# Kernel tuning notes

Hardware: AMD Instinct MI355X
Metric: run time of the kernel (lower is better)

The kernel has to match this reference:

```python
import jax, jax.numpy as jnp
import numpy as np
import math

K_SLOTS = 64
DIM = 512
HEADS = 8
HEAD_DIM = DIM // HEADS
EPS = 1e-20
LN_EPS = 1e-5
SQRT_DIM = 1.0 / math.sqrt(HEAD_DIM)


def layernorm(x, g, b):
    mu = jnp.mean(x, axis=-1, keepdims=True)
    var = jnp.var(x, axis=-1, keepdims=True)
    return (x - mu) * jax.lax.rsqrt(var + LN_EPS) * g + b


def setup_inputs() -> dict:
    key = jax.random.key(0)
    ks = jax.random.split(key, 8)
    B, T = 8, 8192
    lim = 1.0 / math.sqrt(DIM)
    return {
        "X": jax.random.normal(ks[0], (B, T, DIM), jnp.float32),
        "slots_w": jax.random.normal(ks[1], (K_SLOTS, DIM), jnp.float32),
        "g_slots": jnp.ones((DIM,), jnp.float32),
        "b_slots": jnp.zeros((DIM,), jnp.float32),
        "Wk": jax.random.uniform(ks[2], (DIM, DIM), jnp.float32, -lim, lim),
        "bk": jax.random.uniform(ks[3], (DIM,), jnp.float32, -lim, lim),
        "Wv": jax.random.uniform(ks[4], (DIM, DIM), jnp.float32, -lim, lim),
        "bv": jax.random.uniform(ks[5], (DIM,), jnp.float32, -lim, lim),
        "g_after": jnp.ones((DIM,), jnp.float32),
        "b_after": jnp.zeros((DIM,), jnp.float32),
    }


def reference(X, slots_w, g_slots, b_slots, Wk, bk, Wv, bv, g_after, b_after):
    B, T, D = X.shape
    # slots -> queries, shared across batch: (K, D) -> (H, K, hd)
    S = layernorm(slots_w, g_slots, b_slots)
    Q = S.reshape(K_SLOTS, HEADS, HEAD_DIM).transpose(1, 0, 2)  # (H, K, hd)
    # key/value projections, head split: (B, T, D) -> (B, H, T, hd)
    Kx = (X @ Wk.T + bk).reshape(B, T, HEADS, HEAD_DIM).transpose(0, 2, 1, 3)
    V = (X @ Wv.T + bv).reshape(B, T, HEADS, HEAD_DIM).transpose(0, 2, 1, 3)
    # attention logits (B, H, K, T), scale = 1/sqrt(head_dim)
    A = jnp.einsum("hkd,bhsd->bhks", Q, Kx) * SQRT_DIM
    # softmax over the SLOT axis (k), then renormalize by row-sum over s
    W = jax.nn.softmax(A, axis=-2)
    C = jnp.sum(W, axis=-1, keepdims=True)  # (B, H, K, 1)
    A = W / (C + EPS)
    S_hat = jnp.einsum("bhks,bhsd->bhkd", A, V)  # (B, H, K, hd)
    S_hat = S_hat.transpose(0, 2, 1, 3).reshape(B, K_SLOTS, D)
    return layernorm(S_hat, g_after, b_after)
```

## Files before the change

kernel.cpp:

```cpp
#include <hip/hip_runtime.h>
#include <hip/hip_bf16.h>
#include <math.h>

typedef unsigned short ushort_t;
typedef unsigned int u32;

constexpr int D  = 512;
constexpr int T  = 8192;
constexpr int B  = 8;
constexpr int H  = 8;
constexpr int KS = 64;
constexpr int HD = 64;
constexpr float SCALE = 0.125f;
constexpr float LNEPS = 1e-5f;
constexpr float EPS   = 1e-20f;

constexpr int TC  = 128;
constexpr int CPB = 2;

constexpr size_t OFF_S    = 0;
constexpr size_t OFF_BQ   = 32768;
constexpr size_t OFF_SACC = 33280;
constexpr size_t OFF_CACC = 295424;
constexpr size_t OFF_WB2  = 299520;

typedef __attribute__((ext_vector_type(8))) short bf16x8;
typedef __attribute__((ext_vector_type(4))) float f32x4;
typedef __attribute__((ext_vector_type(4))) unsigned short us4;

typedef const __attribute__((address_space(1))) u32* gas_ptr;
typedef __attribute__((address_space(3))) u32* las_ptr;

__device__ __forceinline__ void gload16(const void* g, void* l) {
  __builtin_amdgcn_global_load_lds((gas_ptr)g, (las_ptr)l, 16, 0, 0);
}

__device__ __forceinline__ ushort_t f2bf(float x) {
  __hip_bfloat16 t = __float2bfloat16(x);
  return *(ushort_t*)&t;
}

__device__ __forceinline__ u32 pk2bf(float x, float y) {
  __hip_bfloat162 t = __float22bfloat162_rn(make_float2(x, y));
  return *(u32*)&t;
}

__device__ __forceinline__ bf16x8 cvt8(f32x4 a, f32x4 b) {
  union { bf16x8 v; u32 u[4]; } r;
  r.u[0] = pk2bf(a.x, a.y); r.u[1] = pk2bf(a.z, a.w);
  r.u[2] = pk2bf(b.x, b.y); r.u[3] = pk2bf(b.z, b.w);
  return r.v;
}

__global__ void ln_slots_kernel(const float* __restrict__ slots_w,
                                const float* __restrict__ g, const float* __restrict__ b,
                                const float* __restrict__ bk,
                                float* __restrict__ S, float* __restrict__ bq) {
  __shared__ float red[8];
  int k = blockIdx.x;
  int tid = threadIdx.x;
  float x0 = slots_w[k*D + tid];
  float x1 = slots_w[k*D + tid + 256];
  float s1 = x0 + x1, s2 = x0*x0 + x1*x1;
  for (int off = 32; off; off >>= 1) { s1 += __shfl_xor(s1, off); s2 += __shfl_xor(s2, off); }
  if ((tid & 63) == 0) { red[tid >> 6] = s1; red[4 + (tid >> 6)] = s2; }
  __syncthreads();
  s1 = red[0] + red[1] + red[2] + red[3];
  s2 = red[4] + red[5] + red[6] + red[7];
  float mu = s1 / D;
  float var = s2 / D - mu * mu;
  float rs = rsqrtf(var + LNEPS);
  float y0 = (x0 - mu) * rs * g[tid]       + b[tid];
  float y1 = (x1 - mu) * rs * g[tid + 256] + b[tid + 256];
  S[k*D + tid]       = y0;
  S[k*D + tid + 256] = y1;
  float p0 = y0 * bk[tid];
  float p1 = y1 * bk[tid + 256];
  for (int off = 32; off; off >>= 1) { p0 += __shfl_xor(p0, off); p1 += __shfl_xor(p1, off); }
  if ((tid & 63) == 0) {
    int w = tid >> 6;
    bq[w * KS + k]       = p0 * SCALE;
    bq[(4 + w) * KS + k] = p1 * SCALE;
  }
}

__global__ void setup_kernel(const float* __restrict__ S, const float* __restrict__ Wk,
                             const float* __restrict__ Wv,
                             ushort_t* __restrict__ Wb2, float* __restrict__ Sacc) {
  int id = blockIdx.x;
  int tid = threadIdx.x;
  if (id < 1024) {
    int gid = id * 256 + tid;
    int in = gid & 511;
    int hk = gid >> 9;
    int h = hk >> 6, k = hk & 63;
    const float* srow = S + k*D + h*HD;
    const float* wcol = Wk + (size_t)(h*HD)*D + in;
    float acc = 0.f;
    #pragma unroll 8
    for (int d = 0; d < HD; ++d) acc += srow[d] * wcol[(size_t)d*D];
    Wb2[(size_t)(h*128 + k)*D + in] = f2bf(acc * SCALE);
  } else if (id < 2048) {
    int gid = (id - 1024) * 256 + tid;
    int in = gid & 511;
    int hd = gid >> 9;
    int h = hd >> 6, d = hd & 63;
    Wb2[(size_t)(h*128 + 64 + d)*D + in] = f2bf(Wv[(size_t)hd*D + in]);
  } else {
    int gid = (id - 2048) * 256 + tid;
    if (gid < 266240) Sacc[gid] = 0.f;
  }
}

__global__ __launch_bounds__(256, 3) void main_kernel(
    const float* __restrict__ X, const ushort_t* __restrict__ Wb2,
    const float* __restrict__ bq, const float* __restrict__ bv,
    float* __restrict__ Sacc, float* __restrict__ Cacc) {
  __shared__ __align__(16) char smem[34816];
  float*    A0 = (float*)smem;
  float*    A1 = (float*)(smem + 16384);
  ushort_t* W_lds = (ushort_t*)smem;
  ushort_t* V_lds = (ushort_t*)(smem + 17408);

  const int tid  = threadIdx.x;
  const int lane = tid & 63, w = tid >> 6;
  const int wm = w & 1, wn = w >> 1;
  const int m16 = lane & 15, q = lane >> 4;

  const int id = blockIdx.x;
  const int h  = (id >> 3) & 7;
  const int cg = (id & 7) | ((id >> 6) << 3);
  const int bh = (cg >> 5) * H + h;

  const ushort_t* bp[4];
  #pragma unroll
  for (int j = 0; j < 4; ++j)
    bp[j] = Wb2 + (size_t)(h * 128 + wn * 64 + j * 16 + m16) * D + q * 8;

  f32x4 acc2[4] = {};
  float csum[4] = {0.f, 0.f, 0.f, 0.f};

#define STAGE_A(t, AB) do { \
    _Pragma("unroll") \
    for (int m_ = 0; m_ < 4; ++m_) { \
      int li_ = tid + m_ * 256; \
      int row_ = li_ >> 3, c_ = li_ & 7; \
      gload16(Xc + (size_t)row_ * D + (t) * 32 + ((c_ ^ (row_ & 7)) * 4), \
              (AB) + (size_t)li_ * 4); \
    } \
  } while (0)

#define LOAD_B(t, reg) do { \
    _Pragma("unroll") \
    for (int j_ = 0; j_ < 4; ++j_) reg[j_] = *(const bf16x8*)(bp[j_] + (t) * 32); \
  } while (0)

#define COMPUTE(t, AB, BCUR) do { \
    bf16x8 af_[4]; \
    _Pragma("unroll") \
    for (int i_ = 0; i_ < 4; ++i_) { \
      int r_ = wm * 64 + i_ * 16 + m16; \
      int sw_ = r_ & 7; \
      f32x4 a0_ = *(const f32x4*)((AB) + (size_t)r_ * 32 + (((2 * q)     ^ sw_) * 4)); \
      f32x4 a1_ = *(const f32x4*)((AB) + (size_t)r_ * 32 + (((2 * q + 1) ^ sw_) * 4)); \
      af_[i_] = cvt8(a0_, a1_); \
    } \
    _Pragma("unroll") \
    for (int i_ = 0; i_ < 4; ++i_) \
      _Pragma("unroll") \
      for (int j_ = 0; j_ < 4; ++j_) \
        acc[i_][j_] = __builtin_amdgcn_mfma_f32_16x16x32_bf16(af_[i_], BCUR[j_], acc[i_][j_], 0, 0, 0); \
  } while (0)

#define STEP(t, AB, ABN, BCUR, BNXT) do { \
    if ((t) < 15) { \
      STAGE_A((t) + 1, ABN); \
      LOAD_B((t) + 1, BNXT); \
      asm volatile("s_waitcnt vmcnt(8)" ::: "memory"); \
    } else { \
      asm volatile("s_waitcnt vmcnt(0)" ::: "memory"); \
    } \
    __builtin_amdgcn_s_barrier(); \
    __builtin_amdgcn_sched_barrier(0); \
    COMPUTE(t, AB, BCUR); \
    if ((t) < 15) { \
      __builtin_amdgcn_sched_barrier(0); \
      __builtin_amdgcn_s_barrier(); \
    } \
  } while (0)

  for (int cc = 0; cc < CPB; ++cc) {
    const float* Xc = X + (size_t)(cg * CPB + cc) * TC * D;
    f32x4 acc[4][4] = {};
    bf16x8 bF0[4], bF1[4];

    STAGE_A(0, A0);
    LOAD_B(0, bF0);
    __builtin_amdgcn_sched_barrier(0);

    STEP( 0, A0, A1, bF0, bF1);  STEP( 1, A1, A0, bF1, bF0);
    STEP( 2, A0, A1, bF0, bF1);  STEP( 3, A1, A0, bF1, bF0);
    STEP( 4, A0, A1, bF0, bF1);  STEP( 5, A1, A0, bF1, bF0);
    STEP( 6, A0, A1, bF0, bF1);  STEP( 7, A1, A0, bF1, bF0);
    STEP( 8, A0, A1, bF0, bF1);  STEP( 9, A1, A0, bF1, bF0);
    STEP(10, A0, A1, bF0, bF1);  STEP(11, A1, A0, bF1, bF0);
    STEP(12, A0, A1, bF0, bF1);  STEP(13, A1, A0, bF1, bF0);
    STEP(14, A0, A1, bF0, bF1);  STEP(15, A1, A0, bF1, bF0);

    __syncthreads();

    if (wn == 0) {
      float bqv[4];
      #pragma unroll
      for (int j = 0; j < 4; ++j) bqv[j] = bq[h * KS + j * 16 + m16];
      #pragma unroll
      for (int i = 0; i < 4; ++i) {
        us4 wp[4];
        #pragma unroll
        for (int r = 0; r < 4; ++r) {
          float v0 = acc[i][0][r] + bqv[0];
          float v1 = acc[i][1][r] + bqv[1];
          float v2 = acc[i][2][r] + bqv[2];
          float v3 = acc[i][3][r] + bqv[3];
          float mx = fmaxf(fmaxf(v0, v1), fmaxf(v2, v3));
          mx = fmaxf(mx, __shfl_xor(mx, 1));
          mx = fmaxf(mx, __shfl_xor(mx, 2));
          mx = fmaxf(mx, __shfl_xor(mx, 4));
          mx = fmaxf(mx, __shfl_xor(mx, 8));
          v0 = __expf(v0 - mx); v1 = __expf(v1 - mx);
          v2 = __expf(v2 - mx); v3 = __expf(v3 - mx);
          float s = v0 + v1 + v2 + v3;
          s += __shfl_xor(s, 1); s += __shfl_xor(s, 2);
          s += __shfl_xor(s, 4); s += __shfl_xor(s, 8);
          float inv = __builtin_amdgcn_rcpf(s);
          v0 *= inv; v1 *= inv; v2 *= inv; v3 *= inv;
          csum[0] += v0; csum[1] += v1; csum[2] += v2; csum[3] += v3;
          wp[0][r] = f2bf(v0); wp[1][r] = f2bf(v1);
          wp[2][r] = f2bf(v2); wp[3][r] = f2bf(v3);
        }
        #pragma unroll
        for (int j = 0; j < 4; ++j)
          *(us4*)(W_lds + (j * 16 + m16) * 136 + wm * 64 + i * 16 + q * 4) = wp[j];
      }
    } else {
      float bvv[4];
      #pragma unroll
      for (int j = 0; j < 4; ++j) bvv[j] = bv[h * HD + j * 16 + m16];
      #pragma unroll
      for (int i = 0; i < 4; ++i) {
        #pragma unroll
        for (int j = 0; j < 4; ++j) {
          us4 pk;
          pk.x = f2bf(acc[i][j][0] + bvv[j]);
          pk.y = f2bf(acc[i][j][1] + bvv[j]);
          pk.z = f2bf(acc[i][j][2] + bvv[j]);
          pk.w = f2bf(acc[i][j][3] + bvv[j]);
          *(us4*)(V_lds + (j * 16 + m16) * 136 + wm * 64 + i * 16 + q * 4) = pk;
        }
      }
    }
    __syncthreads();

    #pragma unroll
    for (int kk = 0; kk < 4; ++kk) {
      bf16x8 a = *(const bf16x8*)(W_lds + (w * 16 + m16) * 136 + kk * 32 + q * 8);
      #pragma unroll
      for (int j = 0; j < 4; ++j) {
        bf16x8 bb = *(const bf16x8*)(V_lds + (j * 16 + m16) * 136 + kk * 32 + q * 8);
        acc2[j] = __builtin_amdgcn_mfma_f32_16x16x32_bf16(a, bb, acc2[j], 0, 0, 0);
      }
    }
    __syncthreads();
  }

#undef STEP
#undef COMPUTE
#undef LOAD_B
#undef STAGE_A

  float* Sb = Sacc + (size_t)bh * KS * HD;
  #pragma unroll
  for (int j = 0; j < 4; ++j)
    #pragma unroll
    for (int r = 0; r < 4; ++r)
      atomicAdd(Sb + (w * 16 + q * 4 + r) * HD + j * 16 + m16, acc2[j][r]);

  if (wn == 0) {
    #pragma unroll
    for (int j = 0; j < 4; ++j) {
      float c = csum[j];
      c += __shfl_xor(c, 16);
      c += __shfl_xor(c, 32);
      if (q == 0) atomicAdd(Cacc + (size_t)bh * KS + j * 16 + m16, c);
    }
  }
}

__global__ void finalize_kernel(const float* __restrict__ Sacc, const float* __restrict__ Cacc,
                                const float* __restrict__ g, const float* __restrict__ bb,
                                float* __restrict__ out) {
  __shared__ float red[8];
  int bk_ = blockIdx.x;
  int b = bk_ >> 6, k = bk_ & 63;
  int tid = threadIdx.x;
  float v[2];
  #pragma unroll
  for (int m = 0; m < 2; ++m) {
    int d = tid + m*256;
    int h = d >> 6, dd = d & 63;
    float c = Cacc[((size_t)b*H + h)*KS + k];
    v[m] = Sacc[(((size_t)b*H + h)*KS + k)*HD + dd] / (c + EPS);
  }
  float s1 = v[0] + v[1], s2 = v[0]*v[0] + v[1]*v[1];
  for (int off = 32; off; off >>= 1) { s1 += __shfl_xor(s1, off); s2 += __shfl_xor(s2, off); }
  if ((tid & 63) == 0) { red[tid >> 6] = s1; red[4 + (tid >> 6)] = s2; }
  __syncthreads();
  s1 = red[0] + red[1] + red[2] + red[3];
  s2 = red[4] + red[5] + red[6] + red[7];
  float mu = s1 / D;
  float var = s2 / D - mu * mu;
  float rs = rsqrtf(var + LNEPS);
  #pragma unroll
  for (int m = 0; m < 2; ++m) {
    int d = tid + m*256;
    out[(size_t)bk_*D + d] = (v[m] - mu) * rs * g[d] + bb[d];
  }
}

extern "C" void kernel_launch(void* const* d_in, const int* in_sizes, int n_in,
                              void* d_out, int out_size, void* d_ws, size_t ws_size,
                              hipStream_t stream) {
  const float* X       = (const float*)d_in[0];
  const float* slots_w = (const float*)d_in[1];
  const float* g_slots = (const float*)d_in[2];
  const float* b_slots = (const float*)d_in[3];
  const float* Wk      = (const float*)d_in[4];
  const float* bk      = (const float*)d_in[5];
  const float* Wv      = (const float*)d_in[6];
  const float* bv      = (const float*)d_in[7];
  const float* g_after = (const float*)d_in[8];
  const float* b_after = (const float*)d_in[9];
  float* ws   = (float*)d_ws;
  float* S    = ws + OFF_S;
  float* bq   = ws + OFF_BQ;
  float* Sacc = ws + OFF_SACC;
  float* Cacc = ws + OFF_CACC;
  ushort_t* Wb2 = (ushort_t*)(ws + OFF_WB2);
  float* out  = (float*)d_out;

  hipLaunchKernelGGL(ln_slots_kernel, dim3(64), dim3(256), 0, stream,
                     slots_w, g_slots, b_slots, bk, S, bq);
  hipLaunchKernelGGL(setup_kernel, dim3(3088), dim3(256), 0, stream, S, Wk, Wv, Wb2, Sacc);
  hipLaunchKernelGGL(main_kernel, dim3(2048), dim3(256), 0, stream, X, Wb2, bq, bv, Sacc, Cacc);
  hipLaunchKernelGGL(finalize_kernel, dim3(B * KS), dim3(256), 0, stream,
                     Sacc, Cacc, g_after, b_after, out);
}
```

Baseline: 429.0 us.

## Pre-convert X to bf16 and stage weight tiles through LDS

Adds a pass that converts X to bf16 in the workspace. The main GEMM kernel then streams half the bytes for its A tiles, skips the per-step fp32-to-bf16 conversion, and can raise occupancy to 4 blocks. Weight tiles are now staged into LDS with async global-to-LDS loads instead of per-wave register loads. A fallback kernel keeps fp32 X with LDS-staged weights when the workspace is too small. The extra conversion pass reads all of X and writes a bf16 copy, which adds memory traffic that the main kernel's savings must outweigh.

```diff
diff --git a/kernel.cpp b/kernel.cpp
--- a/kernel.cpp
+++ b/kernel.cpp
@@ -23,6 +23,7 @@
 constexpr size_t OFF_SACC = 33280;
 constexpr size_t OFF_CACC = 295424;
 constexpr size_t OFF_WB2  = 299520;
+constexpr size_t OFF_XB   = 561664;
 
 typedef __attribute__((ext_vector_type(8))) short bf16x8;
 typedef __attribute__((ext_vector_type(4))) float f32x4;
@@ -50,6 +51,17 @@
   r.u[0] = pk2bf(a.x, a.y); r.u[1] = pk2bf(a.z, a.w);
   r.u[2] = pk2bf(b.x, b.y); r.u[3] = pk2bf(b.z, b.w);
   return r.v;
+}
+
+__global__ void xconv_kernel(const float* __restrict__ X, ushort_t* __restrict__ Xb) {
+  int gid = blockIdx.x * 256 + threadIdx.x;
+  #pragma unroll
+  for (int i = 0; i < 8; ++i) {
+    size_t base = ((size_t)i * 524288 + gid) * 8;
+    f32x4 a = *(const f32x4*)(X + base);
+    f32x4 b = *(const f32x4*)(X + base + 4);
+    *(bf16x8*)(Xb + base) = cvt8(a, b);
+  }
 }
 
 __global__ void ln_slots_kernel(const float* __restrict__ slots_w,
@@ -112,13 +124,15 @@
   }
 }
 
-__global__ __launch_bounds__(256, 3) void main_kernel(
-    const float* __restrict__ X, const ushort_t* __restrict__ Wb2,
+__global__ __launch_bounds__(256, 4) void main_kernel_b(
+    const ushort_t* __restrict__ Xb, const ushort_t* __restrict__ Wb2,
     const float* __restrict__ bq, const float* __restrict__ bv,
     float* __restrict__ Sacc, float* __restrict__ Cacc) {
   __shared__ __align__(16) char smem[34816];
-  float*    A0 = (float*)smem;
-  float*    A1 = (float*)(smem + 16384);
+  ushort_t* A0 = (ushort_t*)smem;
+  ushort_t* A1 = (ushort_t*)(smem + 8192);
+  ushort_t* B0 = (ushort_t*)(smem + 16384);
+  ushort_t* B1 = (ushort_t*)(smem + 24576);
   ushort_t* W_lds = (ushort_t*)smem;
   ushort_t* V_lds = (ushort_t*)(smem + 17408);
 
@@ -132,57 +146,63 @@
   const int cg = (id & 7) | ((id >> 6) << 3);
   const int bh = (cg >> 5) * H + h;
 
-  const ushort_t* bp[4];
-  #pragma unroll
-  for (int j = 0; j < 4; ++j)
-    bp[j] = Wb2 + (size_t)(h * 128 + wn * 64 + j * 16 + m16) * D + q * 8;
+  const ushort_t* Wp = Wb2 + (size_t)h * 128 * D;
 
   f32x4 acc2[4] = {};
   float csum[4] = {0.f, 0.f, 0.f, 0.f};
 
 #define STAGE_A(t, AB) do { \
     _Pragma("unroll") \
-    for (int m_ = 0; m_ < 4; ++m_) { \
+    for (int m_ = 0; m_ < 2; ++m_) { \
+      int p_ = tid + m_ * 256;                          \
+      int g_ = (p_ & ~7) | ((p_ & 7) ^ ((p_ >> 3) & 7));  \
+      int row_ = g_ >> 2, c_ = g_ & 3; \
+      gload16(Xc + (size_t)row_ * D + (t) * 32 + c_ * 8, AB + (size_t)p_ * 8); \
+    } \
+  } while (0)
+
+#define STAGE_B(t, BB) do { \
+    _Pragma("unroll") \
+    for (int m_ = 0; m_ < 2; ++m_) { \
       int li_ = tid + m_ * 256; \
-      int row_ = li_ >> 3, c_ = li_ & 7; \
-      gload16(Xc + (size_t)row_ * D + (t) * 32 + ((c_ ^ (row_ & 7)) * 4), \
-              (AB) + (size_t)li_ * 4); \
-    } \
-  } while (0)
-
-#define LOAD_B(t, reg) do { \
-    _Pragma("unroll") \
-    for (int j_ = 0; j_ < 4; ++j_) reg[j_] = *(const bf16x8*)(bp[j_] + (t) * 32); \
-  } while (0)
-
-#define COMPUTE(t, AB, BCUR) do { \
-    bf16x8 af_[4]; \
+      int col_ = li_ >> 2, c_ = li_ & 3; \
+      gload16(Wp + (size_t)col_ * D + (t) * 32 + ((c_ ^ ((col_ >> 1) & 3)) * 8), \
+              BB + (size_t)li_ * 8); \
+    } \
+  } while (0)
+
+#define COMPUTE(t, AB, BB) do { \
+    bf16x8 af_[4], bf_[4]; \
     _Pragma("unroll") \
     for (int i_ = 0; i_ < 4; ++i_) { \
       int r_ = wm * 64 + i_ * 16 + m16; \
-      int sw_ = r_ & 7; \
-      f32x4 a0_ = *(const f32x4*)((AB) + (size_t)r_ * 32 + (((2 * q)     ^ sw_) * 4)); \
-      f32x4 a1_ = *(const f32x4*)((AB) + (size_t)r_ * 32 + (((2 * q + 1) ^ sw_) * 4)); \
-      af_[i_] = cvt8(a0_, a1_); \
+      int g_ = 4 * r_ + q; \
+      int p_ = (g_ & ~7) | ((g_ & 7) ^ ((g_ >> 3) & 7)); \
+      af_[i_] = *(const bf16x8*)(AB + (size_t)p_ * 8); \
+    } \
+    _Pragma("unroll") \
+    for (int j_ = 0; j_ < 4; ++j_) { \
+      int cl_ = wn * 64 + j_ * 16 + m16; \
+      bf_[j_] = *(const bf16x8*)(BB + (size_t)cl_ * 32 + ((q ^ ((cl_ >> 1) & 3)) * 8)); \
     } \
     _Pragma("unroll") \
     for (int i_ = 0; i_ < 4; ++i_) \
       _Pragma("unroll") \
       for (int j_ = 0; j_ < 4; ++j_) \
-        acc[i_][j_] = __builtin_amdgcn_mfma_f32_16x16x32_bf16(af_[i_], BCUR[j_], acc[i_][j_], 0, 0, 0); \
-  } while (0)
-
-#define STEP(t, AB, ABN, BCUR, BNXT) do { \
+        acc[i_][j_] = __builtin_amdgcn_mfma_f32_16x16x32_bf16(af_[i_], bf_[j_], acc[i_][j_], 0, 0, 0); \
+  } while (0)
+
+#define STEP(t, AB, ABN, BB, BBN) do { \
     if ((t) < 15) { \
       STAGE_A((t) + 1, ABN); \
-      LOAD_B((t) + 1, BNXT); \
-      asm volatile("s_waitcnt vmcnt(8)" ::: "memory"); \
+      STAGE_B((t) + 1, BBN); \
+      asm volatile("s_waitcnt vmcnt(4)" ::: "memory"); \
     } else { \
       asm volatile("s_waitcnt vmcnt(0)" ::: "memory"); \
     } \
     __builtin_amdgcn_s_barrier(); \
     __builtin_amdgcn_sched_barrier(0); \
-    COMPUTE(t, AB, BCUR); \
+    COMPUTE(t, AB, BB); \
     if ((t) < 15) { \
       __builtin_amdgcn_sched_barrier(0); \
       __builtin_amdgcn_s_barrier(); \
@@ -190,22 +210,21 @@
   } while (0)
 
   for (int cc = 0; cc < CPB; ++cc) {
-    const float* Xc = X + (size_t)(cg * CPB + cc) * TC * D;
+    const ushort_t* Xc = Xb + (size_t)(cg * CPB + cc) * TC * D;
     f32x4 acc[4][4] = {};
-    bf16x8 bF0[4], bF1[4];
 
     STAGE_A(0, A0);
-    LOAD_B(0, bF0);
+    STAGE_B(0, B0);
     __builtin_amdgcn_sched_barrier(0);
 
-    STEP( 0, A0, A1, bF0, bF1);  STEP( 1, A1, A0, bF1, bF0);
-    STEP( 2, A0, A1, bF0, bF1);  STEP( 3, A1, A0, bF1, bF0);
-    STEP( 4, A0, A1, bF0, bF1);  STEP( 5, A1, A0, bF1, bF0);
-    STEP( 6, A0, A1, bF0, bF1);  STEP( 7, A1, A0, bF1, bF0);
-    STEP( 8, A0, A1, bF0, bF1);  STEP( 9, A1, A0, bF1, bF0);
-    STEP(10, A0, A1, bF0, bF1);  STEP(11, A1, A0, bF1, bF0);
-    STEP(12, A0, A1, bF0, bF1);  STEP(13, A1, A0, bF1, bF0);
-    STEP(14, A0, A1, bF0, bF1);  STEP(15, A1, A0, bF1, bF0);
+    STEP( 0, A0, A1, B0, B1);  STEP( 1, A1, A0, B1, B0);
+    STEP( 2, A0, A1, B0, B1);  STEP( 3, A1, A0, B1, B0);
+    STEP( 4, A0, A1, B0, B1);  STEP( 5, A1, A0, B1, B0);
+    STEP( 6, A0, A1, B0, B1);  STEP( 7, A1, A0, B1, B0);
+    STEP( 8, A0, A1, B0, B1);  STEP( 9, A1, A0, B1, B0);
+    STEP(10, A0, A1, B0, B1);  STEP(11, A1, A0, B1, B0);
+    STEP(12, A0, A1, B0, B1);  STEP(13, A1, A0, B1, B0);
+    STEP(14, A0, A1, B0, B1);  STEP(15, A1, A0, B1, B0);
 
     __syncthreads();
 
@@ -275,8 +294,194 @@
 
 #undef STEP
 #undef COMPUTE
-#undef LOAD_B
+#undef STAGE_B
 #undef STAGE_A
+
+  float* Sb = Sacc + (size_t)bh * KS * HD;
+  #pragma unroll
+  for (int j = 0; j < 4; ++j)
+    #pragma unroll
+    for (int r = 0; r < 4; ++r)
+      atomicAdd(Sb + (w * 16 + q * 4 + r) * HD + j * 16 + m16, acc2[j][r]);
+
+  if (wn == 0) {
+    #pragma unroll
+    for (int j = 0; j < 4; ++j) {
+      float c = csum[j];
+      c += __shfl_xor(c, 16);
+      c += __shfl_xor(c, 32);
+      if (q == 0) atomicAdd(Cacc + (size_t)bh * KS + j * 16 + m16, c);
+    }
+  }
+}
+
+__global__ __launch_bounds__(256, 3) void main_kernel_f(
+    const float* __restrict__ X, const ushort_t* __restrict__ Wb2,
+    const float* __restrict__ bq, const float* __restrict__ bv,
+    float* __restrict__ Sacc, float* __restrict__ Cacc) {
+  __shared__ __align__(16) char smem[49152];
+  float*    A0 = (float*)smem;
+  float*    A1 = (float*)(smem + 16384);
+  ushort_t* B0 = (ushort_t*)(smem + 32768);
+  ushort_t* B1 = (ushort_t*)(smem + 40960);
+  ushort_t* W_lds = (ushort_t*)smem;
+  ushort_t* V_lds = (ushort_t*)(smem + 17408);
+
+  const int tid  = threadIdx.x;
+  const int lane = tid & 63, w = tid >> 6;
+  const int wm = w & 1, wn = w >> 1;
+  const int m16 = lane & 15, q = lane >> 4;
+
+  const int id = blockIdx.x;
+  const int h  = (id >> 3) & 7;
+  const int cg = (id & 7) | ((id >> 6) << 3);
+  const int bh = (cg >> 5) * H + h;
+
+  const ushort_t* Wp = Wb2 + (size_t)h * 128 * D;
+
+  f32x4 acc2[4] = {};
+  float csum[4] = {0.f, 0.f, 0.f, 0.f};
+
+#define F_STAGE(t, AB, BB) do { \
+    _Pragma("unroll") \
+    for (int m_ = 0; m_ < 4; ++m_) { \
+      int li_ = tid + m_ * 256; \
+      int row_ = li_ >> 3, c_ = li_ & 7; \
+      gload16(Xc + (size_t)row_ * D + (t) * 32 + ((c_ ^ (row_ & 7)) * 4), \
+              (AB) + (size_t)li_ * 4); \
+    } \
+    _Pragma("unroll") \
+    for (int m_ = 0; m_ < 2; ++m_) { \
+      int li_ = tid + m_ * 256; \
+      int col_ = li_ >> 2, c_ = li_ & 3; \
+      gload16(Wp + (size_t)col_ * D + (t) * 32 + ((c_ ^ ((col_ >> 1) & 3)) * 8), \
+              (BB) + (size_t)li_ * 8); \
+    } \
+  } while (0)
+
+#define F_COMPUTE(t, AB, BB) do { \
+    bf16x8 af_[4], bf_[4]; \
+    _Pragma("unroll") \
+    for (int i_ = 0; i_ < 4; ++i_) { \
+      int r_ = wm * 64 + i_ * 16 + m16; \
+      int sw_ = r_ & 7; \
+      f32x4 a0_ = *(const f32x4*)((AB) + (size_t)r_ * 32 + (((2 * q)     ^ sw_) * 4)); \
+      f32x4 a1_ = *(const f32x4*)((AB) + (size_t)r_ * 32 + (((2 * q + 1) ^ sw_) * 4)); \
+      af_[i_] = cvt8(a0_, a1_); \
+    } \
+    _Pragma("unroll") \
+    for (int j_ = 0; j_ < 4; ++j_) { \
+      int cl_ = wn * 64 + j_ * 16 + m16; \
+      bf_[j_] = *(const bf16x8*)((BB) + (size_t)cl_ * 32 + ((q ^ ((cl_ >> 1) & 3)) * 8)); \
+    } \
+    _Pragma("unroll") \
+    for (int i_ = 0; i_ < 4; ++i_) \
+      _Pragma("unroll") \
+      for (int j_ = 0; j_ < 4; ++j_) \
+        acc[i_][j_] = __builtin_amdgcn_mfma_f32_16x16x32_bf16(af_[i_], bf_[j_], acc[i_][j_], 0, 0, 0); \
+  } while (0)
+
+#define F_STEP(t, AB, ABN, BB, BBN) do { \
+    if ((t) < 15) { \
+      F_STAGE((t) + 1, ABN, BBN); \
+      asm volatile("s_waitcnt vmcnt(6)" ::: "memory"); \
+    } else { \
+      asm volatile("s_waitcnt vmcnt(0)" ::: "memory"); \
+    } \
+    __builtin_amdgcn_s_barrier(); \
+    __builtin_amdgcn_sched_barrier(0); \
+    F_COMPUTE(t, AB, BB); \
+    if ((t) < 15) { \
+      __builtin_amdgcn_sched_barrier(0); \
+      __builtin_amdgcn_s_barrier(); \
+    } \
+  } while (0)
+
+  for (int cc = 0; cc < CPB; ++cc) {
+    const float* Xc = X + (size_t)(cg * CPB + cc) * TC * D;
+    f32x4 acc[4][4] = {};
+
+    F_STAGE(0, A0, B0);
+    __builtin_amdgcn_sched_barrier(0);
+
+    F_STEP( 0, A0, A1, B0, B1);  F_STEP( 1, A1, A0, B1, B0);
+    F_STEP( 2, A0, A1, B0, B1);  F_STEP( 3, A1, A0, B1, B0);
+    F_STEP( 4, A0, A1, B0, B1);  F_STEP( 5, A1, A0, B1, B0);
+    F_STEP( 6, A0, A1, B0, B1);  F_STEP( 7, A1, A0, B1, B0);
+    F_STEP( 8, A0, A1, B0, B1);  F_STEP( 9, A1, A0, B1, B0);
+    F_STEP(10, A0, A1, B0, B1);  F_STEP(11, A1, A0, B1, B0);
+    F_STEP(12, A0, A1, B0, B1);  F_STEP(13, A1, A0, B1, B0);
+    F_STEP(14, A0, A1, B0, B1);  F_STEP(15, A1, A0, B1, B0);
+
+    __syncthreads();
+
+    if (wn == 0) {
+      float bqv[4];
+      #pragma unroll
+      for (int j = 0; j < 4; ++j) bqv[j] = bq[h * KS + j * 16 + m16];
+      #pragma unroll
+      for (int i = 0; i < 4; ++i) {
+        us4 wp[4];
+        #pragma unroll
+        for (int r = 0; r < 4; ++r) {
+          float v0 = acc[i][0][r] + bqv[0];
+          float v1 = acc[i][1][r] + bqv[1];
+          float v2 = acc[i][2][r] + bqv[2];
+          float v3 = acc[i][3][r] + bqv[3];
+          float mx = fmaxf(fmaxf(v0, v1), fmaxf(v2, v3));
+          mx = fmaxf(mx, __shfl_xor(mx, 1));
+          mx = fmaxf(mx, __shfl_xor(mx, 2));
+          mx = fmaxf(mx, __shfl_xor(mx, 4));
+          mx = fmaxf(mx, __shfl_xor(mx, 8));
+          v0 = __expf(v0 - mx); v1 = __expf(v1 - mx);
+          v2 = __expf(v2 - mx); v3 = __expf(v3 - mx);
+          float s = v0 + v1 + v2 + v3;
+          s += __shfl_xor(s, 1); s += __shfl_xor(s, 2);
+          s += __shfl_xor(s, 4); s += __shfl_xor(s, 8);
+          float inv = __builtin_amdgcn_rcpf(s);
+          v0 *= inv; v1 *= inv; v2 *= inv; v3 *= inv;
+          csum[0] += v0; csum[1] += v1; csum[2] += v2; csum[3] += v3;
+          wp[0][r] = f2bf(v0); wp[1][r] = f2bf(v1);
+          wp[2][r] = f2bf(v2); wp[3][r] = f2bf(v3);
+        }
+        #pragma unroll
+        for (int j = 0; j < 4; ++j)
+          *(us4*)(W_lds + (j * 16 + m16) * 136 + wm * 64 + i * 16 + q * 4) = wp[j];
+      }
+    } else {
+      float bvv[4];
+      #pragma unroll
+      for (int j = 0; j < 4; ++j) bvv[j] = bv[h * HD + j * 16 + m16];
+      #pragma unroll
+      for (int i = 0; i < 4; ++i) {
+        #pragma unroll
+        for (int j = 0; j < 4; ++j) {
+          us4 pk;
+          pk.x = f2bf(acc[i][j][0] + bvv[j]);
+          pk.y = f2bf(acc[i][j][1] + bvv[j]);
+          pk.z = f2bf(acc[i][j][2] + bvv[j]);
+          pk.w = f2bf(acc[i][j][3] + bvv[j]);
+          *(us4*)(V_lds + (j * 16 + m16) * 136 + wm * 64 + i * 16 + q * 4) = pk;
+        }
+      }
+    }
+    __syncthreads();
+
+    #pragma unroll
+    for (int kk = 0; kk < 4; ++kk) {
+      bf16x8 a = *(const bf16x8*)(W_lds + (w * 16 + m16) * 136 + kk * 32 + q * 8);
+      #pragma unroll
+      for (int j = 0; j < 4; ++j) {
+        bf16x8 bb = *(const bf16x8*)(V_lds + (j * 16 + m16) * 136 + kk * 32 + q * 8);
+        acc2[j] = __builtin_amdgcn_mfma_f32_16x16x32_bf16(a, bb, acc2[j], 0, 0, 0);
+      }
+    }
+    __syncthreads();
+  }
+
+#undef F_STEP
+#undef F_COMPUTE
+#undef F_STAGE
 
   float* Sb = Sacc + (size_t)bh * KS * HD;
   #pragma unroll
@@ -346,12 +551,21 @@
   float* Sacc = ws + OFF_SACC;
   float* Cacc = ws + OFF_CACC;
   ushort_t* Wb2 = (ushort_t*)(ws + OFF_WB2);
+  ushort_t* Xb  = (ushort_t*)(ws + OFF_XB);
   float* out  = (float*)d_out;
+
+  const size_t need_bytes = OFF_XB * 4 + (size_t)B * T * D * 2;
+  const bool big_ws = ws_size >= need_bytes;
 
   hipLaunchKernelGGL(ln_slots_kernel, dim3(64), dim3(256), 0, stream,
                      slots_w, g_slots, b_slots, bk, S, bq);
   hipLaunchKernelGGL(setup_kernel, dim3(3088), dim3(256), 0, stream, S, Wk, Wv, Wb2, Sacc);
-  hipLaunchKernelGGL(main_kernel, dim3(2048), dim3(256), 0, stream, X, Wb2, bq, bv, Sacc, Cacc);
+  if (big_ws) {
+    hipLaunchKernelGGL(xconv_kernel, dim3(2048), dim3(256), 0, stream, X, Xb);
+    hipLaunchKernelGGL(main_kernel_b, dim3(2048), dim3(256), 0, stream, Xb, Wb2, bq, bv, Sacc, Cacc);
+  } else {
+    hipLaunchKernelGGL(main_kernel_f, dim3(2048), dim3(256), 0, stream, X, Wb2, bq, bv, Sacc, Cacc);
+  }
   hipLaunchKernelGGL(finalize_kernel, dim3(B * KS), dim3(256), 0, stream,
                      Sacc, Cacc, g_after, b_after, out);
 }
```

Result: faster. 417.1 us (-2.8%).

## Convert X to bf16 in registers before LDS and stage weights through LDS

Applied to the files above, without the earlier changes.

The X tile is now loaded from global into registers, converted to bf16 once per element, and written to swizzled bf16 LDS buffers. Previously the fp32 tile was copied straight to LDS and each wave converted it on every read. The weight tile is also staged through double-buffered LDS with async global loads instead of per-wave direct global reads, and loads for X are issued two steps ahead with a single barrier per step. This halves LDS footprint and traffic for A and removes redundant conversions and duplicate global weight loads, at the cost of more registers for the in-flight X data and tighter dependence on the waitcnt counts being correct.

```diff
diff --git a/kernel.cpp b/kernel.cpp
--- a/kernel.cpp
+++ b/kernel.cpp
@@ -117,10 +117,12 @@
     const float* __restrict__ bq, const float* __restrict__ bv,
     float* __restrict__ Sacc, float* __restrict__ Cacc) {
   __shared__ __align__(16) char smem[34816];
-  float*    A0 = (float*)smem;
-  float*    A1 = (float*)(smem + 16384);
-  ushort_t* W_lds = (ushort_t*)smem;
-  ushort_t* V_lds = (ushort_t*)(smem + 17408);
+  ushort_t* A_lds0 = (ushort_t*)smem;
+  ushort_t* A_lds1 = (ushort_t*)(smem + 8192);
+  ushort_t* B_lds0 = (ushort_t*)(smem + 16384);
+  ushort_t* B_lds1 = (ushort_t*)(smem + 24576);
+  ushort_t* W_lds  = (ushort_t*)smem;
+  ushort_t* V_lds  = (ushort_t*)(smem + 17408);
 
   const int tid  = threadIdx.x;
   const int lane = tid & 63, w = tid >> 6;
@@ -132,80 +134,100 @@
   const int cg = (id & 7) | ((id >> 6) << 3);
   const int bh = (cg >> 5) * H + h;
 
-  const ushort_t* bp[4];
-  #pragma unroll
-  for (int j = 0; j < 4; ++j)
-    bp[j] = Wb2 + (size_t)(h * 128 + wn * 64 + j * 16 + m16) * D + q * 8;
+  const ushort_t* Wp = Wb2 + (size_t)h * 128 * D;
 
   f32x4 acc2[4] = {};
   float csum[4] = {0.f, 0.f, 0.f, 0.f};
 
-#define STAGE_A(t, AB) do { \
+#define GLOAD_A(t, S0, S1, S2, S3) do { \
+    const float* gp_ = Xc + (size_t)(tid >> 1) * D + (t) * 32 + (tid & 1) * 16; \
+    S0 = *(const f32x4*)(gp_);      S1 = *(const f32x4*)(gp_ + 4); \
+    S2 = *(const f32x4*)(gp_ + 8);  S3 = *(const f32x4*)(gp_ + 12); \
+  } while (0)
+
+#define CVT_WRITE(S0, S1, S2, S3, AB) do { \
+    int r_ = tid >> 1, hf_ = tid & 1; \
+    int sw_ = (r_ >> 1) & 3; \
+    bf16x8 lo_ = cvt8(S0, S1); \
+    bf16x8 hi_ = cvt8(S2, S3); \
+    *(bf16x8*)((AB) + r_ * 32 + (((2 * hf_)     ^ sw_) * 8)) = lo_; \
+    *(bf16x8*)((AB) + r_ * 32 + (((2 * hf_ + 1) ^ sw_) * 8)) = hi_; \
+  } while (0)
+
+#define STAGE_B(t, BB) do { \
     _Pragma("unroll") \
-    for (int m_ = 0; m_ < 4; ++m_) { \
+    for (int m_ = 0; m_ < 2; ++m_) { \
       int li_ = tid + m_ * 256; \
-      int row_ = li_ >> 3, c_ = li_ & 7; \
-      gload16(Xc + (size_t)row_ * D + (t) * 32 + ((c_ ^ (row_ & 7)) * 4), \
-              (AB) + (size_t)li_ * 4); \
+      int col_ = li_ >> 2, c_ = li_ & 3; \
+      gload16(Wp + (size_t)col_ * D + (t) * 32 + ((c_ ^ ((col_ >> 1) & 3)) * 8), \
+              (BB) + (size_t)li_ * 8); \
     } \
   } while (0)
 
-#define LOAD_B(t, reg) do { \
-    _Pragma("unroll") \
-    for (int j_ = 0; j_ < 4; ++j_) reg[j_] = *(const bf16x8*)(bp[j_] + (t) * 32); \
-  } while (0)
-
-#define COMPUTE(t, AB, BCUR) do { \
-    bf16x8 af_[4]; \
+#define COMPUTE(t, AB, BB) do { \
+    bf16x8 af_[4], bf_[4]; \
     _Pragma("unroll") \
     for (int i_ = 0; i_ < 4; ++i_) { \
       int r_ = wm * 64 + i_ * 16 + m16; \
-      int sw_ = r_ & 7; \
-      f32x4 a0_ = *(const f32x4*)((AB) + (size_t)r_ * 32 + (((2 * q)     ^ sw_) * 4)); \
-      f32x4 a1_ = *(const f32x4*)((AB) + (size_t)r_ * 32 + (((2 * q + 1) ^ sw_) * 4)); \
-      af_[i_] = cvt8(a0_, a1_); \
+      int sw_ = (r_ >> 1) & 3; \
+      af_[i_] = *(const bf16x8*)((AB) + r_ * 32 + ((q ^ sw_) * 8)); \
+    } \
+    _Pragma("unroll") \
+    for (int j_ = 0; j_ < 4; ++j_) { \
+      int cl_ = wn * 64 + j_ * 16 + m16; \
+      bf_[j_] = *(const bf16x8*)((BB) + (size_t)cl_ * 32 + ((q ^ ((cl_ >> 1) & 3)) * 8)); \
     } \
     _Pragma("unroll") \
     for (int i_ = 0; i_ < 4; ++i_) \
       _Pragma("unroll") \
       for (int j_ = 0; j_ < 4; ++j_) \
-        acc[i_][j_] = __builtin_amdgcn_mfma_f32_16x16x32_bf16(af_[i_], BCUR[j_], acc[i_][j_], 0, 0, 0); \
-  } while (0)
-
-#define STEP(t, AB, ABN, BCUR, BNXT) do { \
-    if ((t) < 15) { \
-      STAGE_A((t) + 1, ABN); \
-      LOAD_B((t) + 1, BNXT); \
-      asm volatile("s_waitcnt vmcnt(8)" ::: "memory"); \
-    } else { \
-      asm volatile("s_waitcnt vmcnt(0)" ::: "memory"); \
-    } \
+        acc[i_][j_] = __builtin_amdgcn_mfma_f32_16x16x32_bf16(af_[i_], bf_[j_], acc[i_][j_], 0, 0, 0); \
+  } while (0)
+
+#define STEP(t, WAITN, AB, ABN, BB, BBN, C0,C1,C2,C3, N0,N1,N2,N3) do { \
+    if ((t) + 2 < 16) { GLOAD_A((t) + 2, N0, N1, N2, N3); } \
+    __builtin_amdgcn_sched_barrier(0); \
+    asm volatile("s_waitcnt vmcnt(" WAITN ")" ::: "memory"); \
+    asm volatile("s_waitcnt lgkmcnt(0)" ::: "memory"); \
     __builtin_amdgcn_s_barrier(); \
     __builtin_amdgcn_sched_barrier(0); \
-    COMPUTE(t, AB, BCUR); \
-    if ((t) < 15) { \
-      __builtin_amdgcn_sched_barrier(0); \
-      __builtin_amdgcn_s_barrier(); \
-    } \
+    if ((t) + 1 < 16) { STAGE_B((t) + 1, BBN); } \
+    COMPUTE(t, AB, BB); \
+    if ((t) + 1 < 16) { CVT_WRITE(C0, C1, C2, C3, ABN); } \
+    __builtin_amdgcn_sched_barrier(0); \
   } while (0)
 
   for (int cc = 0; cc < CPB; ++cc) {
     const float* Xc = X + (size_t)(cg * CPB + cc) * TC * D;
     f32x4 acc[4][4] = {};
-    bf16x8 bF0[4], bF1[4];
-
-    STAGE_A(0, A0);
-    LOAD_B(0, bF0);
+    f32x4 sa0, sa1, sa2, sa3;
+    f32x4 sb0, sb1, sb2, sb3;
+
+    GLOAD_A(0, sa0, sa1, sa2, sa3);
     __builtin_amdgcn_sched_barrier(0);
-
-    STEP( 0, A0, A1, bF0, bF1);  STEP( 1, A1, A0, bF1, bF0);
-    STEP( 2, A0, A1, bF0, bF1);  STEP( 3, A1, A0, bF1, bF0);
-    STEP( 4, A0, A1, bF0, bF1);  STEP( 5, A1, A0, bF1, bF0);
-    STEP( 6, A0, A1, bF0, bF1);  STEP( 7, A1, A0, bF1, bF0);
-    STEP( 8, A0, A1, bF0, bF1);  STEP( 9, A1, A0, bF1, bF0);
-    STEP(10, A0, A1, bF0, bF1);  STEP(11, A1, A0, bF1, bF0);
-    STEP(12, A0, A1, bF0, bF1);  STEP(13, A1, A0, bF1, bF0);
-    STEP(14, A0, A1, bF0, bF1);  STEP(15, A1, A0, bF1, bF0);
+    STAGE_B(0, B_lds0);
+    GLOAD_A(1, sb0, sb1, sb2, sb3);
+    __builtin_amdgcn_sched_barrier(0);
+    asm volatile("s_waitcnt vmcnt(6)" ::: "memory");
+    CVT_WRITE(sa0, sa1, sa2, sa3, A_lds0);
+    __builtin_amdgcn_sched_barrier(0);
+
+    STEP( 0, "4", A_lds0, A_lds1, B_lds0, B_lds1, sb0,sb1,sb2,sb3, sa0,sa1,sa2,sa3);
+    STEP( 1, "4", A_lds1, A_lds0, B_lds1, B_lds0, sa0,sa1,sa2,sa3, sb0,sb1,sb2,sb3);
+    STEP( 2, "4", A_lds0, A_lds1, B_lds0, B_lds1, sb0,sb1,sb2,sb3, sa0,sa1,sa2,sa3);
+    STEP( 3, "4", A_lds1, A_lds0, B_lds1, B_lds0, sa0,sa1,sa2,sa3, sb0,sb1,sb2,sb3);
+    STEP( 4, "4", A_lds0, A_lds1, B_lds0, B_lds1, sb0,sb1,sb2,sb3, sa0,sa1,sa2,sa3);
+    STEP( 5, "4", A_lds1, A_lds0, B_lds1, B_lds0, sa0,sa1,sa2,sa3, sb0,sb1,sb2,sb3);
+    STEP( 6, "4", A_lds0, A_lds1, B_lds0, B_lds1, sb0,sb1,sb2,sb3, sa0,sa1,sa2,sa3);
+    STEP( 7, "4", A_lds1, A_lds0, B_lds1, B_lds0, sa0,sa1,sa2,sa3, sb0,sb1,sb2,sb3);
+    STEP( 8, "4", A_lds0, A_lds1, B_lds0, B_lds1, sb0,sb1,sb2,sb3, sa0,sa1,sa2,sa3);
+    STEP( 9, "4", A_lds1, A_lds0, B_lds1, B_lds0, sa0,sa1,sa2,sa3, sb0,sb1,sb2,sb3);
+    STEP(10, "4", A_lds0, A_lds1, B_lds0, B_lds1, sb0,sb1,sb2,sb3, sa0,sa1,sa2,sa3);
+    STEP(11, "4", A_lds1, A_lds0, B_lds1, B_lds0, sa0,sa1,sa2,sa3, sb0,sb1,sb2,sb3);
+    STEP(12, "4", A_lds0, A_lds1, B_lds0, B_lds1, sb0,sb1,sb2,sb3, sa0,sa1,sa2,sa3);
+    STEP(13, "4", A_lds1, A_lds0, B_lds1, B_lds0, sa0,sa1,sa2,sa3, sb0,sb1,sb2,sb3);
+    STEP(14, "0", A_lds0, A_lds1, B_lds0, B_lds1, sb0,sb1,sb2,sb3, sa0,sa1,sa2,sa3);
+    STEP(15, "0", A_lds1, A_lds0, B_lds1, B_lds0, sa0,sa1,sa2,sa3, sb0,sb1,sb2,sb3);
 
     __syncthreads();
 
@@ -275,8 +297,9 @@
 
 #undef STEP
 #undef COMPUTE
-#undef LOAD_B
-#undef STAGE_A
+#undef STAGE_B
+#undef CVT_WRITE
+#undef GLOAD_A
 
   float* Sb = Sacc + (size_t)bh * KS * HD;
   #pragma unroll
```

Measured after the change: 404.9 us. -5.6%, faster.
